# Performance work log

Hardware: AMD Instinct MI355X
Metric: run time of the kernel (lower is better)

## Reference

```python
import jax, jax.numpy as jnp
import numpy as np

P, S, NOFF, NSTRIP = 192, 36, 72, 71
C, HID = 64, 64
IMG_W, IMG_H = 640.0, 512.0
SAMPLE_X = (np.linspace(0.0, 1.0, S, dtype=np.float32) * NSTRIP).astype(np.int32)  # torch .long() trunc
PRIOR_FEAT_YS = np.ascontiguousarray((1.0 - SAMPLE_X.astype(np.float32) / NSTRIP)[::-1])
PRIOR_YS = np.linspace(1.0, 0.0, NOFF, dtype=np.float32)


def make_priors():
    emb = np.zeros((P, 3), np.float32)
    left = P // 8
    bottom = P * 3 // 4
    strip = 0.5 / (left // 2 - 1)
    bstrip = 1.0 / (bottom // 4 + 1)
    for i in range(left):
        emb[i] = [(i // 2) * strip, 0.0, 0.16 if i % 2 == 0 else 0.32]
    for i in range(left, left + bottom):
        emb[i] = [0.0, ((i - left) // 4 + 1) * bstrip, 0.2 * (i % 4 + 1)]
    for i in range(left + bottom, P):
        emb[i] = [((i - left - bottom) // 2) * strip, 1.0, 0.68 if i % 2 == 0 else 0.84]
    pri = np.zeros((P, 6 + NOFF), np.float32)
    pri[:, 2:5] = emb
    pri[:, 6:] = (emb[:, 1:2] * (IMG_W - 1)
                  + (1.0 - PRIOR_YS[None, :] - emb[:, 0:1]) * IMG_H
                  / np.tan(emb[:, 2:3] * np.pi + 1e-5)) / (IMG_W - 1)
    return pri


def grid_sample_bilinear(feat, gx, gy):
    # feat (B,C,H,W); gx,gy (B,N) in [-1,1]; align_corners=True, zeros padding -> (B,C,N)
    B, Cc, H, W = feat.shape
    x = (gx + 1.0) * 0.5 * (W - 1)
    y = (gy + 1.0) * 0.5 * (H - 1)
    x0 = jnp.floor(x)
    y0 = jnp.floor(y)
    wx = x - x0
    wy = y - y0
    flat = feat.reshape(B, Cc, H * W)

    def tap(ix, iy, wgt):
        valid = ((ix >= 0) & (ix <= W - 1) & (iy >= 0) & (iy <= H - 1)).astype(feat.dtype)
        idx = (jnp.clip(iy, 0, H - 1) * W + jnp.clip(ix, 0, W - 1)).astype(jnp.int32)
        v = jnp.take_along_axis(flat, idx[:, None, :], axis=2)
        return v * (wgt * valid)[:, None, :]

    return (tap(x0, y0, (1 - wx) * (1 - wy)) + tap(x0 + 1, y0, wx * (1 - wy))
            + tap(x0, y0 + 1, (1 - wx) * wy) + tap(x0 + 1, y0 + 1, wx * wy))


def conv1d(x, w, pad):
    # x (N,Cin,L), w (Cout,Cin,K)
    return jax.lax.conv_general_dilated(x, w, window_strides=(1,), padding=[(pad, pad)],
                                        dimension_numbers=('NCH', 'OIH', 'NCH'))


def resize_nearest(x, oh, ow):
    # PyTorch F.interpolate mode='nearest': src = floor(dst*in/out)
    B, Cc, H, W = x.shape
    iy = (np.arange(oh) * H // oh).astype(np.int32)
    ix = (np.arange(ow) * W // ow).astype(np.int32)
    return x[:, :, iy][:, :, :, ix]


def layernorm(x, g, b):
    mu = jnp.mean(x, axis=-1, keepdims=True)
    var = jnp.mean((x - mu) ** 2, axis=-1, keepdims=True)
    return (x - mu) / jnp.sqrt(var + 1e-5) * g + b


def _forward(feat0, feat1, feat2, priors, convs_w, convs_scale, convs_shift,
             cat_w0, cat_w1, cat_w2, cat_scale, cat_shift,
             fkey_w, fkey_scale, fkey_shift, fval_w, fval_b,
             fq_w, fq_b, attW_w, attW_b, fc_w, fc_b, ln_g, ln_b,
             cls_mlp_w, cls_mlp_b, reg_mlp_w, reg_mlp_b,
             cls_head_w, cls_head_b, reg_head_w, reg_head_b):
    feats = [feat0, feat1, feat2]
    cat_ws = [cat_w0, cat_w1, cat_w2]
    B = feat0.shape[0]
    prior_ys = jnp.asarray(PRIOR_YS)
    feat_ys = jnp.asarray(PRIOR_FEAT_YS)
    priors_b = jnp.broadcast_to(priors[None], (B, P, 6 + NOFF))
    priors_on_fm = priors_b[:, :, 6 + SAMPLE_X]
    roi_stages = []
    preds_list = []
    for stage in range(3):
        fmap = feats[stage]
        prior_xs = priors_on_fm[:, :, ::-1]                       # flip sample dim (B,P,S)
        gx = prior_xs.reshape(B, P * S) * 2.0 - 1.0
        gy = jnp.broadcast_to(jnp.tile(feat_ys, P)[None] * 2.0 - 1.0, (B, P * S))
        pooled = grid_sample_bilinear(fmap, gx, gy)               # (B,C,P*S)
        roi = pooled.reshape(B, C, P, S).transpose(0, 2, 1, 3).reshape(B * P, C, S)
        roi_stages.append(roi)
        # ROIGather.roi_fea: per-stage Conv(9)+BN+ReLU then cat + catconv
        cf = [jax.nn.relu(conv1d(roi_stages[i], convs_w[i], 4)
                          * convs_scale[i][None, :, None] + convs_shift[i][None, :, None])
              for i in range(stage + 1)]
        cat = jnp.concatenate(cf, axis=1)
        cat = jax.nn.relu(conv1d(cat, cat_ws[stage], 4)
                          * cat_scale[stage][None, :, None] + cat_shift[stage][None, :, None])
        roi_flat = cat.reshape(B * P, C * S)
        roi_fc = jax.nn.relu(layernorm(roi_flat @ fc_w.T + fc_b, ln_g, ln_b)).reshape(B, P, HID)
        # attention over resized (10x25) feature map
        value = jnp.einsum('bchw,oc->bohw', fmap, fval_w) + fval_b[None, :, None, None]
        value = resize_nearest(value, 10, 25).reshape(B, C, 250)
        keyf = jax.nn.relu(jnp.einsum('bchw,oc->bohw', fmap, fkey_w)
                           * fkey_scale[None, :, None, None] + fkey_shift[None, :, None, None])
        keyf = resize_nearest(keyf, 10, 25).reshape(B, C, 250)
        query = jax.nn.relu(roi_fc * fq_w[None, :, None] + fq_b[None, :, None])  # grouped conv1d
        sim = jax.nn.softmax(jnp.einsum('bpc,bck->bpk', query, keyf) * (C ** -0.5), axis=-1)
        ctx = jnp.einsum('bpk,bck->bpc', sim, value)
        ctx = ctx * attW_w[None, :, None] + attW_b[None, :, None]
        roi_out = roi_fc + ctx                                    # dropout off in eval
        fc_feat = roi_out.reshape(B * P, HID)
        clsf, regf = fc_feat, fc_feat
        for j in range(2):
            clsf = jax.nn.relu(clsf @ cls_mlp_w[j].T + cls_mlp_b[j])
            regf = jax.nn.relu(regf @ reg_mlp_w[j].T + reg_mlp_b[j])
        cls_logits = (clsf @ cls_head_w.T + cls_head_b).reshape(B, P, 2)
        reg = (regf @ reg_head_w.T + reg_head_b).reshape(B, P, NOFF + 4)
        p25 = priors_b[:, :, 2:5] + reg[:, :, :3]
        p5 = reg[:, :, 3:4]
        offs = (p25[:, :, 1:2] * (IMG_W - 1)
                + (1.0 - prior_ys[None, None, :] - p25[:, :, 0:1]) * IMG_H
                / jnp.tan(p25[:, :, 2:3] * np.pi + 1e-5)) / (IMG_W - 1)
        lines = jnp.concatenate([cls_logits, p25, p5, offs], axis=-1)
        preds = jnp.concatenate([cls_logits, p25, p5, offs + reg[:, :, 4:]], axis=-1)
        preds_list.append(preds)
        if stage != 2:
            priors_b = jax.lax.stop_gradient(lines)               # .detach() in torch
            priors_on_fm = priors_b[:, :, 6 + SAMPLE_X]
    return jnp.stack(preds_list)                                  # (3,B,192,78)


def setup_inputs():
    key = jax.random.key(0)
    ks = iter(jax.random.split(key, 40))
    B = 64
    n = lambda shape, s=0.05: jax.random.normal(next(ks), shape, jnp.float32) * s
    return {
        'feat0': n((B, C, 64, 80), 1.0),
        'feat1': n((B, C, 32, 40), 1.0),
        'feat2': n((B, C, 16, 20), 1.0),
        'priors': jnp.asarray(make_priors()),
        'convs_w': n((3, 48, C, 9)),
        'convs_scale': 1.0 + n((3, 48), 0.1),
        'convs_shift': n((3, 48)),
        'cat_w0': n((C, 48, 9)),
        'cat_w1': n((C, 96, 9)),
        'cat_w2': n((C, 144, 9)),
        'cat_scale': 1.0 + n((3, C), 0.1),
        'cat_shift': n((3, C)),
        'fkey_w': n((C, C)),
        'fkey_scale': 1.0 + n((C,), 0.1),
        'fkey_shift': n((C,)),
        'fval_w': n((C, C)),
        'fval_b': n((C,)),
        'fq_w': 1.0 + n((P,), 0.1),
        'fq_b': n((P,)),
        'attW_w': n((P,)),
        'attW_b': n((P,)),
        'fc_w': n((HID, C * S), 0.02),
        'fc_b': n((HID,)),
        'ln_g': 1.0 + n((HID,), 0.1),
        'ln_b': n((HID,)),
        'cls_mlp_w': n((2, HID, HID)),
        'cls_mlp_b': n((2, HID)),
        'reg_mlp_w': n((2, HID, HID)),
        'reg_mlp_b': n((2, HID)),
        'cls_head_w': n((2, HID), 0.001),
        'cls_head_b': n((2,), 0.001),
        'reg_head_w': n((NOFF + 4, HID), 0.001),
        'reg_head_b': n((NOFF + 4,), 0.001),
    }


def reference(feat0, feat1, feat2, priors, convs_w, convs_scale, convs_shift,
              cat_w0, cat_w1, cat_w2, cat_scale, cat_shift,
              fkey_w, fkey_scale, fkey_shift, fval_w, fval_b,
              fq_w, fq_b, attW_w, attW_b, fc_w, fc_b, ln_g, ln_b,
              cls_mlp_w, cls_mlp_b, reg_mlp_w, reg_mlp_b,
              cls_head_w, cls_head_b, reg_head_w, reg_head_b):
    return _forward(feat0, feat1, feat2, priors, convs_w, convs_scale, convs_shift,
                    cat_w0, cat_w1, cat_w2, cat_scale, cat_shift,
                    fkey_w, fkey_scale, fkey_shift, fval_w, fval_b,
                    fq_w, fq_b, attW_w, attW_b, fc_w, fc_b, ln_g, ln_b,
                    cls_mlp_w, cls_mlp_b, reg_mlp_w, reg_mlp_b,
                    cls_head_w, cls_head_b, reg_head_w, reg_head_b)
```

## Files before the change

kernel.cpp:

```cpp
#include <hip/hip_runtime.h>
#include <hip/hip_bf16.h>

#define BB 64
#define PP 192
#define SS 36
#define PI_F 3.14159265358979323846f

typedef __attribute__((ext_vector_type(8))) __bf16 bf16x8;
typedef __attribute__((ext_vector_type(4))) float f32x4;
typedef __attribute__((ext_vector_type(16))) float f32x16;
typedef __attribute__((ext_vector_type(8))) unsigned short us8;

__device__ inline unsigned short f2bf(float f) {
  unsigned int u = __builtin_bit_cast(unsigned int, f);
  unsigned int r = (u + 0x7FFFu + ((u >> 16) & 1u)) >> 16;
  return (unsigned short)r;
}

__device__ inline float bf2f(unsigned short u) {
  return __builtin_bit_cast(float, (unsigned int)u << 16);
}

__device__ inline bf16x8 ld8(const unsigned short* p) {
  us8 v = *(const us8*)p;
// ... 73 lines not shown
                          v = (o < 76) ? f2bf(rhw[o * 64 + c]) : (unsigned short)0; }
    wm[q] = v;
  }
}

__global__ __launch_bounds__(256)
void k_kv(const unsigned short* __restrict__ fmT, int H, int W,
          const float* __restrict__ fkey_w, const float* __restrict__ fkey_scale,
          const float* __restrict__ fkey_shift,
          const float* __restrict__ fval_w, const float* __restrict__ fval_b,
          unsigned short* __restrict__ keyT, unsigned short* __restrict__ valB) {
  __shared__ float pix[64][68];
  __shared__ __align__(16) unsigned short kout[64][80];
  __shared__ __align__(16) unsigned short vout[64][80];
  int tid = threadIdx.x;
  int b = blockIdx.x >> 2;
  int k0 = (blockIdx.x & 3) * 64;

  {
    int key = tid >> 2, cq = tid & 3;
    int k = k0 + key;
    float v[16];
    if (k < 250) {
      int r = k / 25, c2 = k % 25;
      int iy = (r * H) / 10, ix = (c2 * W) / 25;
      const unsigned short* src = fmT + ((size_t)b * H * W + iy * W + ix) * 64 + cq * 16;
      us8 a = *(const us8*)src;
      us8 bb = *(const us8*)(src + 8);
#pragma unroll
      for (int e = 0; e < 8; ++e) { v[e] = bf2f(a[e]); v[8 + e] = bf2f(bb[e]); }
    } else {
#pragma unroll
      for (int e = 0; e < 16; ++e) v[e] = 0.f;
    }
#pragma unroll
    for (int e = 0; e < 16; ++e) pix[key][cq * 16 + e] = v[e];
  }
  __syncthreads();

  {
    int o = tid >> 2, kq = tid & 3;
    float ak[16], av[16];
#pragma unroll
    for (int kk = 0; kk < 16; ++kk) { ak[kk] = 0.f; av[kk] = 0.f; }
    for (int c = 0; c < 64; ++c) {
      float wk = fkey_w[o * 64 + c], wvv = fval_w[o * 64 + c];
#pragma unroll
      for (int kk = 0; kk < 16; ++kk) {
        float pv = pix[kq * 16 + kk][c];
        ak[kk] += pv * wk; av[kk] += pv * wvv;
      }
    }
    float sc_ = fkey_scale[o], sh = fkey_shift[o], vb_ = fval_b[o];
#pragma unroll
    for (int kk = 0; kk < 16; ++kk) {
      int k = kq * 16 + kk;
      float kf = ak[kk] * sc_ + sh; kf = kf > 0.f ? kf : 0.f;
      kout[k][o] = f2bf(kf);
      vout[o][k] = f2bf(av[kk] + vb_);
    }
  }
  __syncthreads();

  {
    int row = tid >> 2, oq = tid & 3;
    *(us8*)(keyT + ((size_t)b * 256 + k0 + row) * 64 + oq * 16)     = *(us8*)&kout[row][oq * 16];
    *(us8*)(keyT + ((size_t)b * 256 + k0 + row) * 64 + oq * 16 + 8) = *(us8*)&kout[row][oq * 16 + 8];
    *(us8*)(valB + ((size_t)b * 64 + row) * 256 + k0 + oq * 16)     = *(us8*)&vout[row][oq * 16];
    *(us8*)(valB + ((size_t)b * 64 + row) * 256 + k0 + oq * 16 + 8) = *(us8*)&vout[row][oq * 16 + 8];
  }
}

template <int STAGE>
__global__ __launch_bounds__(256, 3)
void k_gatherconv(const unsigned short* __restrict__ fmT,
                  const float* __restrict__ priors_cur,
                  const unsigned short* __restrict__ Wr,
                  const float* __restrict__ cscale, const float* __restrict__ cshift,
                  unsigned short* __restrict__ cfg) {
  constexpr int H = (STAGE == 0) ? 64 : (STAGE == 1) ? 32 : 16;
  constexpr int W = (STAGE == 0) ? 80 : (STAGE == 1) ? 40 : 20;
  constexpr int HW = H * W;

  __shared__ float posx[8][36], posy[8][36];
  __shared__ __align__(16) unsigned short Xs[360][64];

  int tid = threadIdx.x;
  int r0 = blockIdx.x * 8;

  for (int idx = tid; idx < 288; idx += 256) {
    int q = idx / 36, j = idx % 36;
    int bp = r0 + q;
    int k = 35 - j;
    int sx = (int)(((float)k / 35.0f) * 71.0f);
    float px = priors_cur[(size_t)bp * 78 + 6 + sx];
    posx[q][j] = px * (float)(W - 1);
    float fy = 1.0f - (float)sx / 71.0f;
    posy[q][j] = fy * (float)(H - 1);
  }
  __syncthreads();

  for (int idx = tid; idx < 360 * 8; idx += 256) {
    int row = idx >> 3, ch8 = idx & 7;
    int p = row - 4;
    unsigned short pk[8] = {0, 0, 0, 0, 0, 0, 0, 0};
    if (p >= 0 && p < 352) {
      int q = p / 44, x = p % 44;
      if (x >= 4 && x < 40) {
        int j = x - 4;
        int b = (r0 + q) / PP;
        float fx = posx[q][j];
        float fy = posy[q][j];
        float x0 = floorf(fx), y0 = floorf(fy);
        float wx = fx - x0, wy = fy - y0;
        float xs2[2] = {x0, x0 + 1.f};
        float ys2[2] = {y0, y0 + 1.f};
        float wxs[2] = {1.f - wx, wx};
        float wys[2] = {1.f - wy, wy};
        float accf[8] = {0.f, 0.f, 0.f, 0.f, 0.f, 0.f, 0.f, 0.f};
#pragma unroll
        for (int ty = 0; ty < 2; ++ty)
#pragma unroll
          for (int tx = 0; tx < 2; ++tx) {
            float xf = xs2[tx], yf = ys2[ty];
            bool v = (xf >= 0.f) && (xf <= (float)(W - 1)) &&
                     (yf >= 0.f) && (yf <= (float)(H - 1));
            int xi = (int)fminf(fmaxf(xf, 0.f), (float)(W - 1));
            int yi = (int)fminf(fmaxf(yf, 0.f), (float)(H - 1));
            float wgt = v ? (wxs[tx] * wys[ty]) : 0.f;
            const us8 vv = *(const us8*)(fmT + ((size_t)b * HW + yi * W + xi) * 64 + ch8 * 8);
#pragma unroll
            for (int e = 0; e < 8; ++e) accf[e] += wgt * bf2f(vv[e]);
          }
#pragma unroll
        for (int e = 0; e < 8; ++e) pk[e] = f2bf(accf[e]);
      }
    }
    int pc = ch8 ^ (row & 7);
    *(us8*)&Xs[row][pc * 8] = *(us8*)pk;
  }
  __syncthreads();

  int wv = tid >> 6, lane = tid & 63, l15 = lane & 15, quad = lane >> 4;
  f32x4 acc[3][6];
#pragma unroll
  for (int m = 0; m < 3; ++m)
#pragma unroll
    for (int s = 0; s < 6; ++s) acc[m][s] = (f32x4)0.f;

#pragma unroll
  for (int k = 0; k < 9; ++k) {
#pragma unroll
    for (int kk = 0; kk < 2; ++kk) {
      bf16x8 af[3];
#pragma unroll
      for (int m = 0; m < 3; ++m)
        af[m] = ld8(Wr + ((size_t)(k * 48 + m * 16 + l15)) * 64 + kk * 32 + quad * 8);
#pragma unroll
      for (int s = 0; s < 6; ++s) {
        int nt = wv + 4 * s;
        if (nt < 22) {
          int row = nt * 16 + l15 + k;
          int pc = (kk * 4 + quad) ^ (row & 7);
          bf16x8 bfr = ld8(&Xs[row][pc * 8]);
#pragma unroll
          for (int m = 0; m < 3; ++m)
            acc[m][s] = __builtin_amdgcn_mfma_f32_16x16x32_bf16(af[m], bfr, acc[m][s], 0, 0, 0);
        }
      }
    }
  }

#pragma unroll
  for (int s = 0; s < 6; ++s) {
    int nt = wv + 4 * s;
    if (nt < 22) {
      int p = nt * 16 + l15;
      int q = p / 44, x = p % 44;
      if (x >= 4 && x < 40) {
        int bp = r0 + q;
#pragma unroll
        for (int m = 0; m < 3; ++m) {
          int o0 = m * 16 + quad * 4;
          unsigned short pk[4];
#pragma unroll
          for (int rg = 0; rg < 4; ++rg) {
            float v = acc[m][s][rg] * cscale[o0 + rg] + cshift[o0 + rg];
            pk[rg] = f2bf(v > 0.f ? v : 0.f);
          }
          *(uint2*)(cfg + ((size_t)bp * 36 + (x - 4)) * 48 + o0) = *(uint2*)pk;
        }
      }
    }
  }
}

template <int STAGE>
__global__ __launch_bounds__(256, 3)
void k_cat(const unsigned short* __restrict__ cfg_all,
           const unsigned short* __restrict__ Wc,
           const float* __restrict__ kscale, const float* __restrict__ kshift,
           unsigned short* __restrict__ catf) {
  constexpr int NC = STAGE + 1;
  __shared__ __align__(16) unsigned short cfs[360][64];
  int tid = threadIdx.x;
  int r0 = blockIdx.x * 8;
  int wv = tid >> 6, lane = tid & 63;
  int l31 = lane & 31, half = lane >> 5;

  int nt0 = wv * 3;
  int ntn = (wv < 3) ? 3 : 2;

  f32x16 acc[2][3];
#pragma unroll
  for (int m = 0; m < 2; ++m)
#pragma unroll
    for (int n = 0; n < 3; ++n) acc[m][n] = (f32x16)0.f;

#pragma unroll
  for (int i = 0; i < NC; ++i) {
    __syncthreads();
    for (int idx = tid; idx < 2160; idx += 256) {
      int row = idx / 6, ch = idx % 6;
      int p = row - 4;
      us8 v = (us8)(unsigned short)0;
      if (p >= 0 && p < 352) {
        int q = p / 44, x = p % 44;
        if (x >= 4 && x < 40) {
          v = *(const us8*)(cfg_all + (size_t)i * (12288ull * 36 * 48) +
                            ((size_t)(r0 + q) * 36 + (x - 4)) * 48 + ch * 8);
        }
      }
      *(us8*)&cfs[row][((ch ^ (row & 7)) * 8)] = v;
    }
    __syncthreads();

#pragma unroll
    for (int t = 0; t < 9; ++t) {
#pragma unroll
      for (int s = 0; s < 3; ++s) {
        int slice_id = i * 27 + t * 3 + s;
        bf16x8 a0 = ld8(Wc + (size_t)(slice_id * 2 + 0) * 512 + lane * 8);
        bf16x8 a1 = ld8(Wc + (size_t)(slice_id * 2 + 1) * 512 + lane * 8);
#pragma unroll
        for (int n = 0; n < 3; ++n) {
          if (n < ntn) {
            int row = (nt0 + n) * 32 + l31 + t;
            int q = (s * 2 + half) ^ (row & 7);
            bf16x8 b = ld8(&cfs[row][q * 8]);
            acc[0][n] = __builtin_amdgcn_mfma_f32_32x32x16_bf16(a0, b, acc[0][n], 0, 0, 0);
            acc[1][n] = __builtin_amdgcn_mfma_f32_32x32x16_bf16(a1, b, acc[1][n], 0, 0, 0);
          }
        }
      }
    }
  }

#pragma unroll
  for (int n = 0; n < 3; ++n) {
    if (n < ntn) {
      int p = (nt0 + n) * 32 + l31;
      int q = p / 44, x = p % 44;
      if (x >= 4 && x < 40) {
        int bp = r0 + q;
        unsigned short* dst = catf + ((size_t)bp * 36 + (x - 4)) * 64;
#pragma unroll
        for (int m = 0; m < 2; ++m) {
#pragma unroll
          for (int r = 0; r < 4; ++r) {
            int o0 = m * 32 + r * 8 + half * 4;
            unsigned short pk[4];
#pragma unroll
            for (int g = 0; g < 4; ++g) {
              int o = o0 + g;
              float v = acc[m][n][r * 4 + g] * kscale[o] + kshift[o];
              pk[g] = f2bf(v > 0.f ? v : 0.f);
            }
            *(uint2*)(dst + o0) = *(uint2*)pk;
          }
        }
      }
    }
  }
}

__global__ __launch_bounds__(64)
void k_fc(const unsigned short* __restrict__ catf,
          const unsigned short* __restrict__ fw,
          const float* __restrict__ fc_b,
          const float* __restrict__ ln_g, const float* __restrict__ ln_b,
          float* __restrict__ roi_fc) {
  __shared__ __align__(16) float fcb[16][68];
  int lane = threadIdx.x, l15 = lane & 15, quad = lane >> 4;
  int nbase = blockIdx.x * 16;

  f32x4 acc[4];
#pragma unroll
  for (int m = 0; m < 4; ++m) acc[m] = (f32x4)0.f;

  for (int ks = 0; ks < 72; ++ks) {
    int j = ks >> 1, ch = (ks & 1) * 32;
    bf16x8 bfr = ld8(catf + ((size_t)(nbase + l15) * 36 + j) * 64 + ch + quad * 8);
#pragma unroll
    for (int m = 0; m < 4; ++m) {
      bf16x8 af = ld8(fw + (size_t)(m * 16 + l15) * 2304 + ks * 32 + quad * 8);
      acc[m] = __builtin_amdgcn_mfma_f32_16x16x32_bf16(af, bfr, acc[m], 0, 0, 0);
    }
  }

#pragma unroll
  for (int m = 0; m < 4; ++m) {
    f32x4 v;
#pragma unroll
    for (int rg = 0; rg < 4; ++rg) v[rg] = acc[m][rg] + fc_b[m * 16 + quad * 4 + rg];
    *(f32x4*)&fcb[l15][m * 16 + quad * 4] = v;
  }
  __syncthreads();

  for (int rr = 0; rr < 16; ++rr) {
    float y = fcb[rr][lane];
    float s = y;
#pragma unroll
    for (int off = 32; off > 0; off >>= 1) s += __shfl_xor(s, off, 64);
    float mu = s * (1.f / 64.f);
    float d = y - mu;
    float v2 = d * d;
#pragma unroll
    for (int off = 32; off > 0; off >>= 1) v2 += __shfl_xor(v2, off, 64);
    float var = v2 * (1.f / 64.f);
    float r = d / sqrtf(var + 1e-5f) * ln_g[lane] + ln_b[lane];
    roi_fc[(size_t)(nbase + rr) * 64 + lane] = r > 0.f ? r : 0.f;
  }
}

__device__ inline f32x4 gemm_tile(const unsigned short* __restrict__ Wrow0,
                                  const unsigned short* Xl, int l15, int quad) {
  f32x4 a = (f32x4)0.f;
#pragma unroll
  for (int kk = 0; kk < 2; ++kk) {
    bf16x8 af = ld8(Wrow0 + (size_t)l15 * 64 + kk * 32 + quad * 8);
    bf16x8 bx = ld8(Xl + l15 * 64 + (((kk * 4 + quad) ^ (l15 & 7)) * 8));
    a = __builtin_amdgcn_mfma_f32_16x16x32_bf16(af, bx, a, 0, 0, 0);
  }
  return a;
}

__global__ __launch_bounds__(64)
void k_att2(const float* __restrict__ roi_fc,
            const unsigned short* __restrict__ keyT,
            const unsigned short* __restrict__ valB,
            const float* __restrict__ fq_w, const float* __restrict__ fq_b,
            const float* __restrict__ attW_w, const float* __restrict__ attW_b,
            const unsigned short* __restrict__ wm,
            const float* __restrict__ cls_mlp_b, const float* __restrict__ reg_mlp_b,
            const float* __restrict__ cls_head_b, const float* __restrict__ reg_head_b,
            const float* __restrict__ priors_cur,
            float* __restrict__ priors_next,
            float* __restrict__ preds) {
  __shared__ __align__(16) unsigned char smem[2048 + 4608 + 8192];
  unsigned short* qx = (unsigned short*)smem;
  unsigned char* Bb = smem + 2048;
  unsigned char* Cb = smem + 2048 + 4608;

  int lane = threadIdx.x;
  int l15 = lane & 15, quad = lane >> 4;
  int rb = blockIdx.x * 16;
  int b = rb / PP;
  int p_base = rb % PP;

  float* rf = (float*)Bb;
  unsigned short* hA = (unsigned short*)Bb;
  unsigned short* hB = (unsigned short*)(Bb + 2304);
  unsigned short* simw = (unsigned short*)Cb;
  unsigned short* rego = (unsigned short*)Cb;
  unsigned short* clso = (unsigned short*)(Cb + 2560);

  for (int it = lane; it < 128; it += 64) {
    int row = it >> 3, ch = it & 7;
    const float* src = roi_fc + (size_t)(rb + row) * 64 + ch * 8;
    float v[8];
#pragma unroll
    for (int e = 0; e < 8; ++e) v[e] = src[e];
#pragma unroll
    for (int e = 0; e < 8; ++e) rf[row * 68 + ch * 8 + e] = v[e];
    int p = p_base + row;
    float qw = fq_w[p], qb = fq_b[p];
    unsigned short pk[8];
#pragma unroll
    for (int e = 0; e < 8; ++e) {
      float q = v[e] * qw + qb;
      pk[e] = f2bf(q > 0.f ? q : 0.f);
    }
    *(us8*)&qx[row * 64 + ((ch ^ (row & 7)) * 8)] = *(us8*)pk;
  }
  __syncthreads();

  f32x4 sc[16];
#pragma unroll
  for (int nt = 0; nt < 16; ++nt) sc[nt] = (f32x4)0.f;
  const unsigned short* kb = keyT + (size_t)b * 256 * 64;
#pragma unroll
  for (int kk = 0; kk < 2; ++kk) {
    bf16x8 af = ld8(&qx[l15 * 64 + (((kk * 4 + quad) ^ (l15 & 7)) * 8)]);
#pragma unroll
    for (int nt = 0; nt < 16; ++nt) {
      bf16x8 bf_ = ld8(kb + (size_t)(nt * 16 + l15) * 64 + kk * 32 + quad * 8);
      sc[nt] = __builtin_amdgcn_mfma_f32_16x16x32_bf16(af, bf_, sc[nt], 0, 0, 0);
    }
  }
  float mx[4] = {-1e30f, -1e30f, -1e30f, -1e30f};
#pragma unroll
  for (int nt = 0; nt < 16; ++nt)
#pragma unroll
    for (int rg = 0; rg < 4; ++rg) {
      float s = sc[nt][rg] * 0.125f;
      if (nt == 15 && l15 >= 10) s = -1e30f;
      sc[nt][rg] = s;
      mx[rg] = fmaxf(mx[rg], s);
    }
#pragma unroll
  for (int rg = 0; rg < 4; ++rg)
#pragma unroll
    for (int off = 1; off < 16; off <<= 1)
      mx[rg] = fmaxf(mx[rg], __shfl_xor(mx[rg], off, 64));
  float sm[4] = {0.f, 0.f, 0.f, 0.f};
#pragma unroll
  for (int nt = 0; nt < 16; ++nt)
#pragma unroll
    for (int rg = 0; rg < 4; ++rg) {
      float e = expf(sc[nt][rg] - mx[rg]);
      sc[nt][rg] = e;
      sm[rg] += e;
    }
#pragma unroll
  for (int rg = 0; rg < 4; ++rg)
#pragma unroll
    for (int off = 1; off < 16; off <<= 1)
      sm[rg] += __shfl_xor(sm[rg], off, 64);
  float rs[4];
#pragma unroll
  for (int rg = 0; rg < 4; ++rg) rs[rg] = 1.f / sm[rg];
#pragma unroll
  for (int nt = 0; nt < 16; ++nt)
#pragma unroll
    for (int rg = 0; rg < 4; ++rg) {
      int row = quad * 4 + rg, col = nt * 16 + l15;
      simw[row * 256 + (((col >> 3) ^ (row & 7)) * 8) + (col & 7)] = f2bf(sc[nt][rg] * rs[rg]);
    }

  f32x4 cv[4];
#pragma unroll
  for (int nt = 0; nt < 4; ++nt) cv[nt] = (f32x4)0.f;
  const unsigned short* vb = valB + (size_t)b * 64 * 256;
#pragma unroll
  for (int ks = 0; ks < 8; ++ks) {
    bf16x8 af = ld8(&simw[l15 * 256 + (((ks * 4 + quad) ^ (l15 & 7)) * 8)]);
#pragma unroll
    for (int nt = 0; nt < 4; ++nt) {
      bf16x8 bf_ = ld8(vb + (size_t)(nt * 16 + l15) * 256 + ks * 32 + quad * 8);
      cv[nt] = __builtin_amdgcn_mfma_f32_16x16x32_bf16(af, bf_, cv[nt], 0, 0, 0);
    }
  }
#pragma unroll
  for (int rg = 0; rg < 4; ++rg) {
    int row = quad * 4 + rg;
    int p = p_base + row;
    float aw = attW_w[p], ab = attW_b[p];
#pragma unroll
    for (int nt = 0; nt < 4; ++nt) {
      int c = nt * 16 + l15;
      float xv = rf[row * 68 + c] + cv[nt][rg] * aw + ab;
      qx[row * 64 + (((c >> 3) ^ (row & 7)) * 8) + (c & 7)] = f2bf(xv);
    }
  }

  const unsigned short* xw = qx;
#pragma unroll
  for (int mt = 0; mt < 4; ++mt) {
// ... 45 lines not shown
  }
#pragma unroll
  for (int mt = 0; mt < 5; ++mt) {
    f32x4 a = gemm_tile(wm + 17408 + mt * 1024, hB, l15, quad);
#pragma unroll
    for (int rg = 0; rg < 4; ++rg) {
      int o = mt * 16 + quad * 4 + rg;
      if (o < 76) rego[l15 * 80 + o] = f2bf(a[rg] + reg_head_b[o]);
    }
  }

  {
    int p_local = lane >> 2, g = lane & 3;
    int bp = rb + p_local;
    const float* pc = priors_cur + (size_t)bp * 78;
    float r0v = bf2f(rego[p_local * 80 + 0]);
    float r1v = bf2f(rego[p_local * 80 + 1]);
    float r2v = bf2f(rego[p_local * 80 + 2]);
    float r3v = bf2f(rego[p_local * 80 + 3]);
    float p0 = pc[2] + r0v;
    float p1 = pc[3] + r1v;
    float p2 = pc[4] + r2v;
    float* po = preds + (size_t)bp * 78;
    float* pn = priors_next ? priors_next + (size_t)bp * 78 : nullptr;
    if (g == 0) {
      float c0v = bf2f(clso[p_local * 2 + 0]);
      float c1v = bf2f(clso[p_local * 2 + 1]);
      po[0] = c0v; po[1] = c1v;
      po[2] = p0; po[3] = p1; po[4] = p2; po[5] = r3v;
      if (pn) { pn[0] = c0v; pn[1] = c1v; pn[2] = p0; pn[3] = p1; pn[4] = p2; pn[5] = r3v; }
    }
    float t = tanf(p2 * PI_F + 1e-5f);
    float inv_t = 512.f / t;
#pragma unroll 2
    for (int i = g * 18; i < g * 18 + 18; ++i) {
      float py = 1.0f - (float)i / 71.0f;
      float offs = (p1 * 639.0f + (1.0f - py - p0) * inv_t) * (1.0f / 639.0f);
      po[6 + i] = offs + bf2f(rego[p_local * 80 + 4 + i]);
      if (pn) pn[6 + i] = offs;
    }
  }
}

extern "C" void kernel_launch(void* const* d_in, const int* in_sizes, int n_in,
                              void* d_out, int out_size, void* d_ws, size_t ws_size,
                              hipStream_t stream) {
  (void)in_sizes; (void)n_in; (void)out_size; (void)ws_size;
  const float* feat[3] = {(const float*)d_in[0], (const float*)d_in[1], (const float*)d_in[2]};
  const float* priors      = (const float*)d_in[3];
  const float* convs_w     = (const float*)d_in[4];
  const float* convs_scale = (const float*)d_in[5];
  const float* convs_shift = (const float*)d_in[6];
  const float* cat_w[3]    = {(const float*)d_in[7], (const float*)d_in[8], (const float*)d_in[9]};
  const float* cat_scale   = (const float*)d_in[10];
  const float* cat_shift   = (const float*)d_in[11];
  const float* fkey_w      = (const float*)d_in[12];
  const float* fkey_scale  = (const float*)d_in[13];
  const float* fkey_shift  = (const float*)d_in[14];
  const float* fval_w      = (const float*)d_in[15];
  const float* fval_b      = (const float*)d_in[16];
  const float* fq_w        = (const float*)d_in[17];
  const float* fq_b        = (const float*)d_in[18];
  const float* attW_w      = (const float*)d_in[19];
  const float* attW_b      = (const float*)d_in[20];
  const float* fc_w        = (const float*)d_in[21];
  const float* fc_b        = (const float*)d_in[22];
  const float* ln_g        = (const float*)d_in[23];
  const float* ln_b        = (const float*)d_in[24];
  const float* cls_mlp_w   = (const float*)d_in[25];
  const float* cls_mlp_b   = (const float*)d_in[26];
  const float* reg_mlp_w   = (const float*)d_in[27];
  const float* reg_mlp_b   = (const float*)d_in[28];
  const float* cls_head_w  = (const float*)d_in[29];
  const float* cls_head_b  = (const float*)d_in[30];
  const float* reg_head_w  = (const float*)d_in[31];
  const float* reg_head_b  = (const float*)d_in[32];
  float* out = (float*)d_out;

  char* wp = (char*)d_ws;
  auto alloc = [&](size_t bytes) { char* r = wp; wp += (bytes + 255) & ~(size_t)255; return r; };

  float* priA   = (float*)alloc((size_t)BB * PP * 78 * 4);
  float* priB   = (float*)alloc((size_t)BB * PP * 78 * 4);
  float* roi_fc = (float*)alloc((size_t)BB * PP * 64 * 4);
  unsigned short* keyT = (unsigned short*)alloc((size_t)BB * 256 * 64 * 2);
  unsigned short* valB = (unsigned short*)alloc((size_t)BB * 64 * 256 * 2);
  unsigned short* Wr   = (unsigned short*)alloc(82944ull * 2);
  unsigned short* Wc   = (unsigned short*)alloc(165888ull * 2);
  unsigned short* fw   = (unsigned short*)alloc(147456ull * 2);
  unsigned short* wm   = (unsigned short*)alloc(22528ull * 2);
  unsigned short* cfg  = (unsigned short*)alloc(3ull * 12288 * 36 * 48 * 2);
  unsigned short* catf = (unsigned short*)alloc(12288ull * 36 * 64 * 2);
  unsigned short* fmT  = (unsigned short*)alloc((size_t)BB * 64 * 80 * 64 * 2);

  const int HW[3][2] = {{64, 80}, {32, 40}, {16, 20}};
  const size_t wcoff[3] = {0, 27648, 82944};

  k_init_priors<<<dim3((BB * PP * 78 + 255) / 256), dim3(256), 0, stream>>>(priors, priA);
  k_repack<<<dim3((418816 + 255) / 256), dim3(256), 0, stream>>>(
      convs_w, cat_w[0], cat_w[1], cat_w[2], fc_w,
      cls_mlp_w, reg_mlp_w, cls_head_w, reg_head_w, Wr, Wc, fw, wm);

  float* pcur = priA;
  float* pnext = priB;
  for (int s = 0; s < 3; ++s) {
    int H = HW[s][0], W = HW[s][1];
    int hw = H * W;
    int tiles = hw / 64;
    k_transpose<<<dim3(BB * tiles), dim3(256), 0, stream>>>(feat[s], hw, tiles, fmT);

    k_kv<<<dim3(BB * 4), dim3(256), 0, stream>>>(
        fmT, H, W, fkey_w, fkey_scale, fkey_shift, fval_w, fval_b, keyT, valB);

    if (s == 0) {
      k_gatherconv<0><<<dim3(1536), dim3(256), 0, stream>>>(
          fmT, pcur, Wr + 0 * 27648, convs_scale + 0, convs_shift + 0,
          cfg + 0ull * 12288 * 36 * 48);
      k_cat<0><<<dim3(1536), dim3(256), 0, stream>>>(
          cfg, Wc + wcoff[0], cat_scale + 0, cat_shift + 0, catf);
    } else if (s == 1) {
      k_gatherconv<1><<<dim3(1536), dim3(256), 0, stream>>>(
          fmT, pcur, Wr + 1 * 27648, convs_scale + 48, convs_shift + 48,
          cfg + 1ull * 12288 * 36 * 48);
      k_cat<1><<<dim3(1536), dim3(256), 0, stream>>>(
          cfg, Wc + wcoff[1], cat_scale + 64, cat_shift + 64, catf);
    } else {
      k_gatherconv<2><<<dim3(1536), dim3(256), 0, stream>>>(
          fmT, pcur, Wr + 2 * 27648, convs_scale + 96, convs_shift + 96,
          cfg + 2ull * 12288 * 36 * 48);
      k_cat<2><<<dim3(1536), dim3(256), 0, stream>>>(
          cfg, Wc + wcoff[2], cat_scale + 128, cat_shift + 128, catf);
    }

    k_fc<<<dim3(768), dim3(64), 0, stream>>>(catf, fw, fc_b, ln_g, ln_b, roi_fc);

    k_att2<<<dim3(768), dim3(64), 0, stream>>>(
        roi_fc, keyT, valB, fq_w, fq_b, attW_w, attW_b, wm,
        cls_mlp_b, reg_mlp_b, cls_head_b, reg_head_b,
        pcur, (s < 2) ? pnext : (float*)nullptr,
        out + (size_t)s * BB * PP * 78);

    float* tmp = pcur; pcur = pnext; pnext = tmp;
  }
}
```

Before: 929.7 us.

## Fuse fc+layernorm into attention kernel and make conv/cat waves independent

The fc GEMM and layernorm kernel is merged into the attention kernel, which drops one launch and the fp32 roi_fc round trip through global memory. In the gather-conv and cat kernels each wave now handles two priors with its own shared-memory slice, so block-wide __syncthreads are gone and the padding logic is simpler. In exchange, each wave computes 96 padded columns for 88 useful ones, and shared memory grows slightly (392 rows instead of 360). The fused kernel relies on the wave-local LDS writes in fcb being visible without a barrier, which is safe for a single 64-thread wave.

```diff
diff --git a/kernel.cpp b/kernel.cpp
--- a/kernel.cpp
+++ b/kernel.cpp
@@ -179,35 +179,35 @@
   constexpr int W = (STAGE == 0) ? 80 : (STAGE == 1) ? 40 : 20;
   constexpr int HW = H * W;
 
-  __shared__ float posx[8][36], posy[8][36];
-  __shared__ __align__(16) unsigned short Xs[360][64];
+  __shared__ __align__(16) unsigned short Xs[392][64];
+  __shared__ float posx[4][2][36], posy[4][2][36];
 
   int tid = threadIdx.x;
-  int r0 = blockIdx.x * 8;
-
-  for (int idx = tid; idx < 288; idx += 256) {
-    int q = idx / 36, j = idx % 36;
-    int bp = r0 + q;
+  int wv = tid >> 6, lane = tid & 63;
+  int l15 = lane & 15, quad = lane >> 4;
+  int r0 = blockIdx.x * 8 + wv * 2;
+  unsigned short* my = &Xs[wv * 96][0];
+
+  for (int it = lane; it < 72; it += 64) {
+    int q = it / 36, j = it % 36;
     int k = 35 - j;
     int sx = (int)(((float)k / 35.0f) * 71.0f);
-    float px = priors_cur[(size_t)bp * 78 + 6 + sx];
-    posx[q][j] = px * (float)(W - 1);
-    float fy = 1.0f - (float)sx / 71.0f;
-    posy[q][j] = fy * (float)(H - 1);
-  }
-  __syncthreads();
-
-  for (int idx = tid; idx < 360 * 8; idx += 256) {
-    int row = idx >> 3, ch8 = idx & 7;
+    float px = priors_cur[(size_t)(r0 + q) * 78 + 6 + sx];
+    posx[wv][q][j] = px * (float)(W - 1);
+    posy[wv][q][j] = (1.0f - (float)sx / 71.0f) * (float)(H - 1);
+  }
+
+  for (int it = lane; it < 768; it += 64) {
+    int row = it >> 3, ch8 = it & 7;
     int p = row - 4;
     unsigned short pk[8] = {0, 0, 0, 0, 0, 0, 0, 0};
-    if (p >= 0 && p < 352) {
+    if (p >= 0 && p < 88) {
       int q = p / 44, x = p % 44;
       if (x >= 4 && x < 40) {
         int j = x - 4;
         int b = (r0 + q) / PP;
-        float fx = posx[q][j];
-        float fy = posy[q][j];
+        float fx = posx[wv][q][j];
+        float fy = posy[wv][q][j];
         float x0 = floorf(fx), y0 = floorf(fy);
         float wx = fx - x0, wy = fy - y0;
         float xs2[2] = {x0, x0 + 1.f};
@@ -233,17 +233,14 @@
         for (int e = 0; e < 8; ++e) pk[e] = f2bf(accf[e]);
       }
     }
-    int pc = ch8 ^ (row & 7);
-    *(us8*)&Xs[row][pc * 8] = *(us8*)pk;
-  }
-  __syncthreads();
-
-  int wv = tid >> 6, lane = tid & 63, l15 = lane & 15, quad = lane >> 4;
+    *(us8*)&my[row * 64 + (((ch8 ^ (row & 7))) * 8)] = *(us8*)pk;
+  }
+
   f32x4 acc[3][6];
 #pragma unroll
   for (int m = 0; m < 3; ++m)
 #pragma unroll
-    for (int s = 0; s < 6; ++s) acc[m][s] = (f32x4)0.f;
+    for (int n = 0; n < 6; ++n) acc[m][n] = (f32x4)0.f;
 
 #pragma unroll
   for (int k = 0; k < 9; ++k) {
@@ -254,25 +251,21 @@
       for (int m = 0; m < 3; ++m)
         af[m] = ld8(Wr + ((size_t)(k * 48 + m * 16 + l15)) * 64 + kk * 32 + quad * 8);
 #pragma unroll
-      for (int s = 0; s < 6; ++s) {
-        int nt = wv + 4 * s;
-        if (nt < 22) {
-          int row = nt * 16 + l15 + k;
-          int pc = (kk * 4 + quad) ^ (row & 7);
-          bf16x8 bfr = ld8(&Xs[row][pc * 8]);
-#pragma unroll
-          for (int m = 0; m < 3; ++m)
-            acc[m][s] = __builtin_amdgcn_mfma_f32_16x16x32_bf16(af[m], bfr, acc[m][s], 0, 0, 0);
-        }
+      for (int n = 0; n < 6; ++n) {
+        int row = n * 16 + l15 + k;
+        int pc = (kk * 4 + quad) ^ (row & 7);
+        bf16x8 bfr = ld8(&my[row * 64 + pc * 8]);
+#pragma unroll
+        for (int m = 0; m < 3; ++m)
+          acc[m][n] = __builtin_amdgcn_mfma_f32_16x16x32_bf16(af[m], bfr, acc[m][n], 0, 0, 0);
       }
     }
   }
 
 #pragma unroll
-  for (int s = 0; s < 6; ++s) {
-    int nt = wv + 4 * s;
-    if (nt < 22) {
-      int p = nt * 16 + l15;
+  for (int n = 0; n < 6; ++n) {
+    int p = n * 16 + l15;
+    if (p < 88) {
       int q = p / 44, x = p % 44;
       if (x >= 4 && x < 40) {
         int bp = r0 + q;
@@ -282,7 +275,7 @@
           unsigned short pk[4];
 #pragma unroll
           for (int rg = 0; rg < 4; ++rg) {
-            float v = acc[m][s][rg] * cscale[o0 + rg] + cshift[o0 + rg];
+            float v = acc[m][n][rg] * cscale[o0 + rg] + cshift[o0 + rg];
             pk[rg] = f2bf(v > 0.f ? v : 0.f);
           }
           *(uint2*)(cfg + ((size_t)bp * 36 + (x - 4)) * 48 + o0) = *(uint2*)pk;
@@ -299,14 +292,17 @@
            const float* __restrict__ kscale, const float* __restrict__ kshift,
            unsigned short* __restrict__ catf) {
   constexpr int NC = STAGE + 1;
-  __shared__ __align__(16) unsigned short cfs[360][64];
+  __shared__ __align__(16) unsigned short cfs[392][64];
   int tid = threadIdx.x;
-  int r0 = blockIdx.x * 8;
   int wv = tid >> 6, lane = tid & 63;
   int l31 = lane & 31, half = lane >> 5;
-
-  int nt0 = wv * 3;
-  int ntn = (wv < 3) ? 3 : 2;
+  int r0 = blockIdx.x * 8 + wv * 2;
+  unsigned short* my = &cfs[wv * 96][0];
+
+  for (int it = lane; it < 192; it += 64) {
+    int row = it >> 1, ch = 6 + (it & 1);
+    *(us8*)&my[row * 64 + ((ch ^ (row & 7)) * 8)] = (us8)(unsigned short)0;
+  }
 
   f32x16 acc[2][3];
 #pragma unroll
@@ -316,21 +312,19 @@
 
 #pragma unroll
   for (int i = 0; i < NC; ++i) {
-    __syncthreads();
-    for (int idx = tid; idx < 2160; idx += 256) {
-      int row = idx / 6, ch = idx % 6;
+    for (int it = lane; it < 576; it += 64) {
+      int row = it / 6, ch = it % 6;
       int p = row - 4;
       us8 v = (us8)(unsigned short)0;
-      if (p >= 0 && p < 352) {
+      if (p >= 0 && p < 88) {
         int q = p / 44, x = p % 44;
         if (x >= 4 && x < 40) {
           v = *(const us8*)(cfg_all + (size_t)i * (12288ull * 36 * 48) +
                             ((size_t)(r0 + q) * 36 + (x - 4)) * 48 + ch * 8);
         }
       }
-      *(us8*)&cfs[row][((ch ^ (row & 7)) * 8)] = v;
-    }
-    __syncthreads();
+      *(us8*)&my[row * 64 + ((ch ^ (row & 7)) * 8)] = v;
+    }
 
 #pragma unroll
     for (int t = 0; t < 9; ++t) {
@@ -341,13 +335,11 @@
         bf16x8 a1 = ld8(Wc + (size_t)(slice_id * 2 + 1) * 512 + lane * 8);
 #pragma unroll
         for (int n = 0; n < 3; ++n) {
-          if (n < ntn) {
-            int row = (nt0 + n) * 32 + l31 + t;
-            int q = (s * 2 + half) ^ (row & 7);
-            bf16x8 b = ld8(&cfs[row][q * 8]);
-            acc[0][n] = __builtin_amdgcn_mfma_f32_32x32x16_bf16(a0, b, acc[0][n], 0, 0, 0);
-            acc[1][n] = __builtin_amdgcn_mfma_f32_32x32x16_bf16(a1, b, acc[1][n], 0, 0, 0);
-          }
+          int row = n * 32 + l31 + t;
+          int q = (s * 2 + half) ^ (row & 7);
+          bf16x8 b = ld8(&my[row * 64 + q * 8]);
+          acc[0][n] = __builtin_amdgcn_mfma_f32_32x32x16_bf16(a0, b, acc[0][n], 0, 0, 0);
+          acc[1][n] = __builtin_amdgcn_mfma_f32_32x32x16_bf16(a1, b, acc[1][n], 0, 0, 0);
         }
       }
     }
@@ -355,8 +347,8 @@
 
 #pragma unroll
   for (int n = 0; n < 3; ++n) {
-    if (n < ntn) {
-      int p = (nt0 + n) * 32 + l31;
+    int p = n * 32 + l31;
+    if (p < 88) {
       int q = p / 44, x = p % 44;
       if (x >= 4 && x < 40) {
         int bp = r0 + q;
@@ -381,55 +373,6 @@
   }
 }
 
-__global__ __launch_bounds__(64)
-void k_fc(const unsigned short* __restrict__ catf,
-          const unsigned short* __restrict__ fw,
-          const float* __restrict__ fc_b,
-          const float* __restrict__ ln_g, const float* __restrict__ ln_b,
-          float* __restrict__ roi_fc) {
-  __shared__ __align__(16) float fcb[16][68];
-  int lane = threadIdx.x, l15 = lane & 15, quad = lane >> 4;
-  int nbase = blockIdx.x * 16;
-
-  f32x4 acc[4];
-#pragma unroll
-  for (int m = 0; m < 4; ++m) acc[m] = (f32x4)0.f;
-
-  for (int ks = 0; ks < 72; ++ks) {
-    int j = ks >> 1, ch = (ks & 1) * 32;
-    bf16x8 bfr = ld8(catf + ((size_t)(nbase + l15) * 36 + j) * 64 + ch + quad * 8);
-#pragma unroll
-    for (int m = 0; m < 4; ++m) {
-      bf16x8 af = ld8(fw + (size_t)(m * 16 + l15) * 2304 + ks * 32 + quad * 8);
-      acc[m] = __builtin_amdgcn_mfma_f32_16x16x32_bf16(af, bfr, acc[m], 0, 0, 0);
-    }
-  }
-
-#pragma unroll
-  for (int m = 0; m < 4; ++m) {
-    f32x4 v;
-#pragma unroll
-    for (int rg = 0; rg < 4; ++rg) v[rg] = acc[m][rg] + fc_b[m * 16 + quad * 4 + rg];
-    *(f32x4*)&fcb[l15][m * 16 + quad * 4] = v;
-  }
-  __syncthreads();
-
-  for (int rr = 0; rr < 16; ++rr) {
-    float y = fcb[rr][lane];
-    float s = y;
-#pragma unroll
-    for (int off = 32; off > 0; off >>= 1) s += __shfl_xor(s, off, 64);
-    float mu = s * (1.f / 64.f);
-    float d = y - mu;
-    float v2 = d * d;
-#pragma unroll
-    for (int off = 32; off > 0; off >>= 1) v2 += __shfl_xor(v2, off, 64);
-    float var = v2 * (1.f / 64.f);
-    float r = d / sqrtf(var + 1e-5f) * ln_g[lane] + ln_b[lane];
-    roi_fc[(size_t)(nbase + rr) * 64 + lane] = r > 0.f ? r : 0.f;
-  }
-}
-
 __device__ inline f32x4 gemm_tile(const unsigned short* __restrict__ Wrow0,
                                   const unsigned short* Xl, int l15, int quad) {
   f32x4 a = (f32x4)0.f;
@@ -443,17 +386,20 @@
 }
 
 __global__ __launch_bounds__(64)
-void k_att2(const float* __restrict__ roi_fc,
-            const unsigned short* __restrict__ keyT,
-            const unsigned short* __restrict__ valB,
-            const float* __restrict__ fq_w, const float* __restrict__ fq_b,
-            const float* __restrict__ attW_w, const float* __restrict__ attW_b,
-            const unsigned short* __restrict__ wm,
-            const float* __restrict__ cls_mlp_b, const float* __restrict__ reg_mlp_b,
-            const float* __restrict__ cls_head_b, const float* __restrict__ reg_head_b,
-            const float* __restrict__ priors_cur,
-            float* __restrict__ priors_next,
-            float* __restrict__ preds) {
+void k_fc_att(const unsigned short* __restrict__ catf,
+              const unsigned short* __restrict__ fw,
+              const float* __restrict__ fc_b,
+              const float* __restrict__ ln_g, const float* __restrict__ ln_b,
+              const unsigned short* __restrict__ keyT,
+              const unsigned short* __restrict__ valB,
+              const float* __restrict__ fq_w, const float* __restrict__ fq_b,
+              const float* __restrict__ attW_w, const float* __restrict__ attW_b,
+              const unsigned short* __restrict__ wm,
+              const float* __restrict__ cls_mlp_b, const float* __restrict__ reg_mlp_b,
+              const float* __restrict__ cls_head_b, const float* __restrict__ reg_head_b,
+              const float* __restrict__ priors_cur,
+              float* __restrict__ priors_next,
+              float* __restrict__ preds) {
   __shared__ __align__(16) unsigned char smem[2048 + 4608 + 8192];
   unsigned short* qx = (unsigned short*)smem;
   unsigned char* Bb = smem + 2048;
@@ -468,29 +414,52 @@
   float* rf = (float*)Bb;
   unsigned short* hA = (unsigned short*)Bb;
   unsigned short* hB = (unsigned short*)(Bb + 2304);
+  float* fcb = (float*)Cb;
   unsigned short* simw = (unsigned short*)Cb;
   unsigned short* rego = (unsigned short*)Cb;
   unsigned short* clso = (unsigned short*)(Cb + 2560);
 
-  for (int it = lane; it < 128; it += 64) {
-    int row = it >> 3, ch = it & 7;
-    const float* src = roi_fc + (size_t)(rb + row) * 64 + ch * 8;
-    float v[8];
-#pragma unroll
-    for (int e = 0; e < 8; ++e) v[e] = src[e];
-#pragma unroll
-    for (int e = 0; e < 8; ++e) rf[row * 68 + ch * 8 + e] = v[e];
-    int p = p_base + row;
-    float qw = fq_w[p], qb = fq_b[p];
-    unsigned short pk[8];
-#pragma unroll
-    for (int e = 0; e < 8; ++e) {
-      float q = v[e] * qw + qb;
-      pk[e] = f2bf(q > 0.f ? q : 0.f);
-    }
-    *(us8*)&qx[row * 64 + ((ch ^ (row & 7)) * 8)] = *(us8*)pk;
-  }
-  __syncthreads();
+  {
+    f32x4 acc[4];
+#pragma unroll
+    for (int m = 0; m < 4; ++m) acc[m] = (f32x4)0.f;
+    for (int ks = 0; ks < 72; ++ks) {
+      int j = ks >> 1, ch = (ks & 1) * 32;
+      bf16x8 bfr = ld8(catf + ((size_t)(rb + l15) * 36 + j) * 64 + ch + quad * 8);
+#pragma unroll
+      for (int m = 0; m < 4; ++m) {
+        bf16x8 af = ld8(fw + (size_t)(m * 16 + l15) * 2304 + ks * 32 + quad * 8);
+        acc[m] = __builtin_amdgcn_mfma_f32_16x16x32_bf16(af, bfr, acc[m], 0, 0, 0);
+      }
+    }
+#pragma unroll
+    for (int m = 0; m < 4; ++m) {
+      f32x4 v;
+#pragma unroll
+      for (int rg = 0; rg < 4; ++rg) v[rg] = acc[m][rg] + fc_b[m * 16 + quad * 4 + rg];
+      *(f32x4*)&fcb[l15 * 68 + m * 16 + quad * 4] = v;
+    }
+  }
+
+  for (int rr = 0; rr < 16; ++rr) {
+    float y = fcb[rr * 68 + lane];
+    float s = y;
+#pragma unroll
+    for (int off = 32; off > 0; off >>= 1) s += __shfl_xor(s, off, 64);
+    float mu = s * (1.f / 64.f);
+    float d = y - mu;
+    float v2 = d * d;
+#pragma unroll
+    for (int off = 32; off > 0; off >>= 1) v2 += __shfl_xor(v2, off, 64);
+    float var = v2 * (1.f / 64.f);
+    float r = d / sqrtf(var + 1e-5f) * ln_g[lane] + ln_b[lane];
+    r = r > 0.f ? r : 0.f;
+    rf[rr * 68 + lane] = r;
+    int p = p_base + rr;
+    float q = r * fq_w[p] + fq_b[p];
+    q = q > 0.f ? q : 0.f;
+    qx[rr * 64 + (((lane >> 3) ^ (rr & 7)) * 8) + (lane & 7)] = f2bf(q);
+  }
 
   f32x4 sc[16];
 #pragma unroll
@@ -702,7 +671,6 @@
 
   float* priA   = (float*)alloc((size_t)BB * PP * 78 * 4);
   float* priB   = (float*)alloc((size_t)BB * PP * 78 * 4);
-  float* roi_fc = (float*)alloc((size_t)BB * PP * 64 * 4);
   unsigned short* keyT = (unsigned short*)alloc((size_t)BB * 256 * 64 * 2);
   unsigned short* valB = (unsigned short*)alloc((size_t)BB * 64 * 256 * 2);
   unsigned short* Wr   = (unsigned short*)alloc(82944ull * 2);
@@ -752,10 +720,8 @@
           cfg, Wc + wcoff[2], cat_scale + 128, cat_shift + 128, catf);
     }
 
-    k_fc<<<dim3(768), dim3(64), 0, stream>>>(catf, fw, fc_b, ln_g, ln_b, roi_fc);
-
-    k_att2<<<dim3(768), dim3(64), 0, stream>>>(
-        roi_fc, keyT, valB, fq_w, fq_b, attW_w, attW_b, wm,
+    k_fc_att<<<dim3(768), dim3(64), 0, stream>>>(
+        catf, fw, fc_b, ln_g, ln_b, keyT, valB, fq_w, fq_b, attW_w, attW_b, wm,
         cls_mlp_b, reg_mlp_b, cls_head_b, reg_head_b,
         pcur, (s < 2) ? pnext : (float*)nullptr,
         out + (size_t)s * BB * PP * 78);
```

Result: no change. 932.2 us (+0.3%).

## Fuse fc+layernorm into attention kernel and software-pipeline conv MFMA operand loads

Applied to the files above, without the earlier changes.

Merges the fc GEMM plus LayerNorm kernel into the attention kernel, so the roi_fc activations stay in shared memory instead of going through a global buffer. This also removes one launch per stage. Separately, the gather-conv and cat-conv inner loops now prefetch the next step's weight and LDS operands into registers before issuing the current MFMAs, to hide load latency. The cost is higher register pressure. The fused kernel writes fcb into shared memory and has no __syncthreads before the cross-lane reads, which relies on the block being a single wave.

```diff
diff --git a/kernel.cpp b/kernel.cpp
--- a/kernel.cpp
+++ b/kernel.cpp
@@ -245,26 +245,36 @@
 #pragma unroll
     for (int s = 0; s < 6; ++s) acc[m][s] = (f32x4)0.f;
 
-#pragma unroll
-  for (int k = 0; k < 9; ++k) {
-#pragma unroll
-    for (int kk = 0; kk < 2; ++kk) {
-      bf16x8 af[3];
+  bf16x8 afc[3];
+#pragma unroll
+  for (int m = 0; m < 3; ++m)
+    afc[m] = ld8(Wr + ((size_t)(0 * 48 + m * 16 + l15)) * 64 + 0 * 32 + quad * 8);
+
+#pragma unroll
+  for (int step = 0; step < 18; ++step) {
+    int k = step >> 1, kk = step & 1;
+    bf16x8 afn[3];
+    if (step < 17) {
+      int k2 = (step + 1) >> 1, kk2 = (step + 1) & 1;
 #pragma unroll
       for (int m = 0; m < 3; ++m)
-        af[m] = ld8(Wr + ((size_t)(k * 48 + m * 16 + l15)) * 64 + kk * 32 + quad * 8);
-#pragma unroll
-      for (int s = 0; s < 6; ++s) {
-        int nt = wv + 4 * s;
-        if (nt < 22) {
-          int row = nt * 16 + l15 + k;
-          int pc = (kk * 4 + quad) ^ (row & 7);
-          bf16x8 bfr = ld8(&Xs[row][pc * 8]);
-#pragma unroll
-          for (int m = 0; m < 3; ++m)
-            acc[m][s] = __builtin_amdgcn_mfma_f32_16x16x32_bf16(af[m], bfr, acc[m][s], 0, 0, 0);
-        }
-      }
+        afn[m] = ld8(Wr + ((size_t)(k2 * 48 + m * 16 + l15)) * 64 + kk2 * 32 + quad * 8);
+    }
+#pragma unroll
+    for (int s = 0; s < 6; ++s) {
+      int nt = wv + 4 * s;
+      if (nt < 22) {
+        int row = nt * 16 + l15 + k;
+        int pc = (kk * 4 + quad) ^ (row & 7);
+        bf16x8 bfr = ld8(&Xs[row][pc * 8]);
+#pragma unroll
+        for (int m = 0; m < 3; ++m)
+          acc[m][s] = __builtin_amdgcn_mfma_f32_16x16x32_bf16(afc[m], bfr, acc[m][s], 0, 0, 0);
+      }
+    }
+    if (step < 17) {
+#pragma unroll
+      for (int m = 0; m < 3; ++m) afc[m] = afn[m];
     }
   }
 
@@ -332,23 +342,49 @@
     }
     __syncthreads();
 
-#pragma unroll
-    for (int t = 0; t < 9; ++t) {
-#pragma unroll
-      for (int s = 0; s < 3; ++s) {
-        int slice_id = i * 27 + t * 3 + s;
-        bf16x8 a0 = ld8(Wc + (size_t)(slice_id * 2 + 0) * 512 + lane * 8);
-        bf16x8 a1 = ld8(Wc + (size_t)(slice_id * 2 + 1) * 512 + lane * 8);
+    bf16x8 a0c, a1c, bc[3];
+    {
+      int sid = i * 27;
+      a0c = ld8(Wc + (size_t)(sid * 2 + 0) * 512 + lane * 8);
+      a1c = ld8(Wc + (size_t)(sid * 2 + 1) * 512 + lane * 8);
+#pragma unroll
+      for (int n = 0; n < 3; ++n) {
+        if (n < ntn) {
+          int row = (nt0 + n) * 32 + l31;
+          int q = half ^ (row & 7);
+          bc[n] = ld8(&cfs[row][q * 8]);
+        }
+      }
+    }
+
+#pragma unroll
+    for (int u = 0; u < 27; ++u) {
+      bf16x8 a0n, a1n, bn[3];
+      if (u < 26) {
+        int u2 = u + 1, t2 = u2 / 3, s2 = u2 % 3;
+        int sid2 = i * 27 + u2;
+        a0n = ld8(Wc + (size_t)(sid2 * 2 + 0) * 512 + lane * 8);
+        a1n = ld8(Wc + (size_t)(sid2 * 2 + 1) * 512 + lane * 8);
 #pragma unroll
         for (int n = 0; n < 3; ++n) {
           if (n < ntn) {
-            int row = (nt0 + n) * 32 + l31 + t;
-            int q = (s * 2 + half) ^ (row & 7);
-            bf16x8 b = ld8(&cfs[row][q * 8]);
-            acc[0][n] = __builtin_amdgcn_mfma_f32_32x32x16_bf16(a0, b, acc[0][n], 0, 0, 0);
-            acc[1][n] = __builtin_amdgcn_mfma_f32_32x32x16_bf16(a1, b, acc[1][n], 0, 0, 0);
+            int row = (nt0 + n) * 32 + l31 + t2;
+            int q = (s2 * 2 + half) ^ (row & 7);
+            bn[n] = ld8(&cfs[row][q * 8]);
           }
         }
+      }
+#pragma unroll
+      for (int n = 0; n < 3; ++n) {
+        if (n < ntn) {
+          acc[0][n] = __builtin_amdgcn_mfma_f32_32x32x16_bf16(a0c, bc[n], acc[0][n], 0, 0, 0);
+          acc[1][n] = __builtin_amdgcn_mfma_f32_32x32x16_bf16(a1c, bc[n], acc[1][n], 0, 0, 0);
+        }
+      }
+      if (u < 26) {
+        a0c = a0n; a1c = a1n;
+#pragma unroll
+        for (int n = 0; n < 3; ++n) bc[n] = bn[n];
       }
     }
   }
@@ -381,55 +417,6 @@
   }
 }
 
-__global__ __launch_bounds__(64)
-void k_fc(const unsigned short* __restrict__ catf,
-          const unsigned short* __restrict__ fw,
-          const float* __restrict__ fc_b,
-          const float* __restrict__ ln_g, const float* __restrict__ ln_b,
-          float* __restrict__ roi_fc) {
-  __shared__ __align__(16) float fcb[16][68];
-  int lane = threadIdx.x, l15 = lane & 15, quad = lane >> 4;
-  int nbase = blockIdx.x * 16;
-
-  f32x4 acc[4];
-#pragma unroll
-  for (int m = 0; m < 4; ++m) acc[m] = (f32x4)0.f;
-
-  for (int ks = 0; ks < 72; ++ks) {
-    int j = ks >> 1, ch = (ks & 1) * 32;
-    bf16x8 bfr = ld8(catf + ((size_t)(nbase + l15) * 36 + j) * 64 + ch + quad * 8);
-#pragma unroll
-    for (int m = 0; m < 4; ++m) {
-      bf16x8 af = ld8(fw + (size_t)(m * 16 + l15) * 2304 + ks * 32 + quad * 8);
-      acc[m] = __builtin_amdgcn_mfma_f32_16x16x32_bf16(af, bfr, acc[m], 0, 0, 0);
-    }
-  }
-
-#pragma unroll
-  for (int m = 0; m < 4; ++m) {
-    f32x4 v;
-#pragma unroll
-    for (int rg = 0; rg < 4; ++rg) v[rg] = acc[m][rg] + fc_b[m * 16 + quad * 4 + rg];
-    *(f32x4*)&fcb[l15][m * 16 + quad * 4] = v;
-  }
-  __syncthreads();
-
-  for (int rr = 0; rr < 16; ++rr) {
-    float y = fcb[rr][lane];
-    float s = y;
-#pragma unroll
-    for (int off = 32; off > 0; off >>= 1) s += __shfl_xor(s, off, 64);
-    float mu = s * (1.f / 64.f);
-    float d = y - mu;
-    float v2 = d * d;
-#pragma unroll
-    for (int off = 32; off > 0; off >>= 1) v2 += __shfl_xor(v2, off, 64);
-    float var = v2 * (1.f / 64.f);
-    float r = d / sqrtf(var + 1e-5f) * ln_g[lane] + ln_b[lane];
-    roi_fc[(size_t)(nbase + rr) * 64 + lane] = r > 0.f ? r : 0.f;
-  }
-}
-
 __device__ inline f32x4 gemm_tile(const unsigned short* __restrict__ Wrow0,
                                   const unsigned short* Xl, int l15, int quad) {
   f32x4 a = (f32x4)0.f;
@@ -443,17 +430,20 @@
 }
 
 __global__ __launch_bounds__(64)
-void k_att2(const float* __restrict__ roi_fc,
-            const unsigned short* __restrict__ keyT,
-            const unsigned short* __restrict__ valB,
-            const float* __restrict__ fq_w, const float* __restrict__ fq_b,
-            const float* __restrict__ attW_w, const float* __restrict__ attW_b,
-            const unsigned short* __restrict__ wm,
-            const float* __restrict__ cls_mlp_b, const float* __restrict__ reg_mlp_b,
-            const float* __restrict__ cls_head_b, const float* __restrict__ reg_head_b,
-            const float* __restrict__ priors_cur,
-            float* __restrict__ priors_next,
-            float* __restrict__ preds) {
+void k_fc_att(const unsigned short* __restrict__ catf,
+              const unsigned short* __restrict__ fw,
+              const float* __restrict__ fc_b,
+              const float* __restrict__ ln_g, const float* __restrict__ ln_b,
+              const unsigned short* __restrict__ keyT,
+              const unsigned short* __restrict__ valB,
+              const float* __restrict__ fq_w, const float* __restrict__ fq_b,
+              const float* __restrict__ attW_w, const float* __restrict__ attW_b,
+              const unsigned short* __restrict__ wm,
+              const float* __restrict__ cls_mlp_b, const float* __restrict__ reg_mlp_b,
+              const float* __restrict__ cls_head_b, const float* __restrict__ reg_head_b,
+              const float* __restrict__ priors_cur,
+              float* __restrict__ priors_next,
+              float* __restrict__ preds) {
   __shared__ __align__(16) unsigned char smem[2048 + 4608 + 8192];
   unsigned short* qx = (unsigned short*)smem;
   unsigned char* Bb = smem + 2048;
@@ -468,29 +458,52 @@
   float* rf = (float*)Bb;
   unsigned short* hA = (unsigned short*)Bb;
   unsigned short* hB = (unsigned short*)(Bb + 2304);
+  float* fcb = (float*)Cb;
   unsigned short* simw = (unsigned short*)Cb;
   unsigned short* rego = (unsigned short*)Cb;
   unsigned short* clso = (unsigned short*)(Cb + 2560);
 
-  for (int it = lane; it < 128; it += 64) {
-    int row = it >> 3, ch = it & 7;
-    const float* src = roi_fc + (size_t)(rb + row) * 64 + ch * 8;
-    float v[8];
-#pragma unroll
-    for (int e = 0; e < 8; ++e) v[e] = src[e];
-#pragma unroll
-    for (int e = 0; e < 8; ++e) rf[row * 68 + ch * 8 + e] = v[e];
-    int p = p_base + row;
-    float qw = fq_w[p], qb = fq_b[p];
-    unsigned short pk[8];
-#pragma unroll
-    for (int e = 0; e < 8; ++e) {
-      float q = v[e] * qw + qb;
-      pk[e] = f2bf(q > 0.f ? q : 0.f);
-    }
-    *(us8*)&qx[row * 64 + ((ch ^ (row & 7)) * 8)] = *(us8*)pk;
-  }
-  __syncthreads();
+  {
+    f32x4 acc[4];
+#pragma unroll
+    for (int m = 0; m < 4; ++m) acc[m] = (f32x4)0.f;
+    for (int ks = 0; ks < 72; ++ks) {
+      int j = ks >> 1, ch = (ks & 1) * 32;
+      bf16x8 bfr = ld8(catf + ((size_t)(rb + l15) * 36 + j) * 64 + ch + quad * 8);
+#pragma unroll
+      for (int m = 0; m < 4; ++m) {
+        bf16x8 af = ld8(fw + (size_t)(m * 16 + l15) * 2304 + ks * 32 + quad * 8);
+        acc[m] = __builtin_amdgcn_mfma_f32_16x16x32_bf16(af, bfr, acc[m], 0, 0, 0);
+      }
+    }
+#pragma unroll
+    for (int m = 0; m < 4; ++m) {
+      f32x4 v;
+#pragma unroll
+      for (int rg = 0; rg < 4; ++rg) v[rg] = acc[m][rg] + fc_b[m * 16 + quad * 4 + rg];
+      *(f32x4*)&fcb[l15 * 68 + m * 16 + quad * 4] = v;
+    }
+  }
+
+  for (int rr = 0; rr < 16; ++rr) {
+    float y = fcb[rr * 68 + lane];
+    float s = y;
+#pragma unroll
+    for (int off = 32; off > 0; off >>= 1) s += __shfl_xor(s, off, 64);
+    float mu = s * (1.f / 64.f);
+    float d = y - mu;
+    float v2 = d * d;
+#pragma unroll
+    for (int off = 32; off > 0; off >>= 1) v2 += __shfl_xor(v2, off, 64);
+    float var = v2 * (1.f / 64.f);
+    float r = d / sqrtf(var + 1e-5f) * ln_g[lane] + ln_b[lane];
+    r = r > 0.f ? r : 0.f;
+    rf[rr * 68 + lane] = r;
+    int p = p_base + rr;
+    float q = r * fq_w[p] + fq_b[p];
+    q = q > 0.f ? q : 0.f;
+    qx[rr * 64 + (((lane >> 3) ^ (rr & 7)) * 8) + (lane & 7)] = f2bf(q);
+  }
 
   f32x4 sc[16];
 #pragma unroll
@@ -702,7 +715,6 @@
 
   float* priA   = (float*)alloc((size_t)BB * PP * 78 * 4);
   float* priB   = (float*)alloc((size_t)BB * PP * 78 * 4);
-  float* roi_fc = (float*)alloc((size_t)BB * PP * 64 * 4);
   unsigned short* keyT = (unsigned short*)alloc((size_t)BB * 256 * 64 * 2);
   unsigned short* valB = (unsigned short*)alloc((size_t)BB * 64 * 256 * 2);
   unsigned short* Wr   = (unsigned short*)alloc(82944ull * 2);
@@ -752,10 +764,8 @@
           cfg, Wc + wcoff[2], cat_scale + 128, cat_shift + 128, catf);
     }
 
-    k_fc<<<dim3(768), dim3(64), 0, stream>>>(catf, fw, fc_b, ln_g, ln_b, roi_fc);
-
-    k_att2<<<dim3(768), dim3(64), 0, stream>>>(
-        roi_fc, keyT, valB, fq_w, fq_b, attW_w, attW_b, wm,
+    k_fc_att<<<dim3(768), dim3(64), 0, stream>>>(
+        catf, fw, fc_b, ln_g, ln_b, keyT, valB, fq_w, fq_b, attW_w, attW_b, wm,
         cls_mlp_b, reg_mlp_b, cls_head_b, reg_head_b,
         pcur, (s < 2) ? pnext : (float*)nullptr,
         out + (size_t)s * BB * PP * 78);
```

After: 894.5 us. 3.8% less time.
